# Kernel tuning notes

Hardware: AMD Instinct MI355X
Metric: run time of the kernel (lower is better)

## Reference

```python
import jax, jax.numpy as jnp
import numpy as np


def _gcn_conv(x, W, b, src, dst, n_nodes):
    """PyG-style GCNConv: XW, symmetric deg^-1/2 normalization over edges
    (with self-loops already included in src/dst), scatter-add to targets, + bias."""
    xw = x @ W  # [N, F_out]
    ones = jnp.ones(src.shape[0], dtype=xw.dtype)
    deg = jax.ops.segment_sum(ones, dst, num_segments=n_nodes)  # in-degree incl. self-loops
    dinv = jnp.where(deg > 0, jax.lax.rsqrt(jnp.maximum(deg, 1.0)), 0.0)
    norm = dinv[src] * dinv[dst]                        # [E]
    msgs = xw[src] * norm[:, None]                      # [E, F_out] gather + scale
    out = jax.ops.segment_sum(msgs, dst, num_segments=n_nodes)  # scatter-add
    return out + b


def setup_inputs() -> dict:
    key = jax.random.key(0)
    k1, k2, k3, k4 = jax.random.split(key, 4)
    N, E = 100000, 1600000
    IN, HID, OUT = 128, 64, 64
    x = jax.random.normal(k1, (N, IN), dtype=jnp.float32)
    edge_index = jax.random.randint(k2, (2, E), 0, N, dtype=jnp.int64)
    W1 = jax.random.normal(k3, (IN, HID), dtype=jnp.float32) * (1.0 / np.sqrt(IN))
    b1 = jnp.zeros((HID,), dtype=jnp.float32)
    W2 = jax.random.normal(k4, (HID, OUT), dtype=jnp.float32) * (1.0 / np.sqrt(HID))
    b2 = jnp.zeros((OUT,), dtype=jnp.float32)
    return {"x": x, "edge_index": edge_index, "W1": W1, "b1": b1, "W2": W2, "b2": b2}


def reference(x, edge_index, W1, b1, W2, b2):
    n_nodes = x.shape[0]
    # add self-loops (PyG GCNConv default add_self_loops=True)
    loops = jnp.arange(n_nodes, dtype=edge_index.dtype)
    src = jnp.concatenate([edge_index[0], loops])
    dst = jnp.concatenate([edge_index[1], loops])
    h = _gcn_conv(x, W1, b1, src, dst, n_nodes)
    h = jax.nn.relu(h)
    z = _gcn_conv(h, W2, b2, src, dst, n_nodes)
    return z
```

## Files before the change

kernel.cpp:

```cpp
#include <hip/hip_runtime.h>

#define IN_F 128
#define HID_F 64
#define BKT_SHIFT 9
#define BKT_SIZE 512
#define CHUNK 4096

typedef unsigned short ushort_t;
typedef __attribute__((ext_vector_type(8))) short bf16x8;
typedef __attribute__((ext_vector_type(8))) unsigned short u16x8;
typedef __attribute__((ext_vector_type(4))) float f32x4;

__device__ inline ushort_t f2bf(float f) {
    unsigned u = __float_as_uint(f);
    u += 0x7FFFu + ((u >> 16) & 1u);
    return (ushort_t)(u >> 16);
}
__device__ inline float bf2f(ushort_t u) {
    return __uint_as_float((unsigned)u << 16);
}


__global__ __launch_bounds__(256) void k_hist_pack(const int* __restrict__ dst,
        int* __restrict__ ghist, int E, int nbE,
        const float* __restrict__ W1, const float* __restrict__ W2,
        ushort_t* __restrict__ Bp1, ushort_t* __restrict__ Bp2) {
    int tid = threadIdx.x;
    if ((int)blockIdx.x >= nbE) {
        int id = ((int)blockIdx.x - nbE) * 256 + tid;
        int iw = (id < 8192) ? id : id - 8192;
        int j = iw & 7, lane = (iw >> 3) & 63, t = (iw >> 9) & 3, s = iw >> 11;
        int k = s * 32 + ((lane >> 4) << 3) + j;
        int n = t * 16 + (lane & 15);
        if (id < 8192)        Bp1[iw] = f2bf(W1[k * 64 + n]);
        else if (id < 12288)  Bp2[iw] = f2bf(W2[k * 64 + n]);
        return;
    }
    __shared__ int hist[256];
    hist[tid] = 0;
    __syncthreads();
    int e0 = blockIdx.x * CHUNK, e1 = min(e0 + CHUNK, E);
    for (int e = e0 + tid; e < e1; e += 256)
        atomicAdd(&hist[dst[e] >> BKT_SHIFT], 1);
    __syncthreads();
    ghist[blockIdx.x * 256 + tid] = hist[tid];
}

__global__ __launch_bounds__(256) void k_colscan(int* __restrict__ ghist,
        int* __restrict__ gcount, int nb) {
    __shared__ int s[256];
    int t = threadIdx.x;
    int b = blockIdx.x;
    int j0 = 2 * t, j1 = 2 * t + 1;
    int v0 = (j0 < nb) ? ghist[j0 * 256 + b] : 0;
    int v1 = (j1 < nb) ? ghist[j1 * 256 + b] : 0;
    int p = v0 + v1;
    s[t] = p;
    __syncthreads();
    for (int off = 1; off < 256; off <<= 1) {
        int v = (t >= off) ? s[t - off] : 0;
        __syncthreads();
        s[t] += v;
        __syncthreads();
    }
    int excl = s[t] - p;
    if (j0 < nb) ghist[j0 * 256 + b] = excl;
    if (j1 < nb) ghist[j1 * 256 + b] = excl + v0;
    if (t == 255) gcount[b] = s[255];
}

__global__ __launch_bounds__(256) void k_scatter(const int* __restrict__ src,
        const int* __restrict__ dst, const int* __restrict__ ghist,
        const int* __restrict__ gcount, unsigned* __restrict__ gbin, int E) {
    __shared__ int cur[256];
    __shared__ int s[256];
    int tid = threadIdx.x;
    int gc = gcount[tid];
    s[tid] = gc;
    __syncthreads();
    for (int off = 1; off < 256; off <<= 1) {
        int v = (tid >= off) ? s[tid - off] : 0;
        __syncthreads();
        s[tid] += v;
        __syncthreads();
    }
    cur[tid] = ghist[blockIdx.x * 256 + tid] + (s[tid] - gc);
    __syncthreads();
    int e0 = blockIdx.x * CHUNK, e1 = min(e0 + CHUNK, E);
    for (int e = e0 + tid; e < e1; e += 256) {
        int d = dst[e];
        int b = d >> BKT_SHIFT;
        int p = atomicAdd(&cur[b], 1);
        gbin[p] = ((unsigned)(d & (BKT_SIZE - 1)) << 23) | (unsigned)src[e];
    }
}

__global__ __launch_bounds__(256) void k_fill2(const unsigned* __restrict__ gbin,
        const int* __restrict__ gcount, int* __restrict__ rowptr,
        float* __restrict__ dinv, int* __restrict__ col, int N, int E) {
    __shared__ int cnt[4096];
    __shared__ int s[256];
    int tid = threadIdx.x;
    int b = blockIdx.x;
    int gc = gcount[tid];
    s[tid] = gc;
    __syncthreads();
    for (int off = 1; off < 256; off <<= 1) {
        int v = (tid >= off) ? s[tid - off] : 0;
        __syncthreads();
        s[tid] += v;
        __syncthreads();
    }
    int e0 = (b > 0) ? s[b - 1] : 0;
    int e1 = s[b];
    if (b == 0 && tid == 0) rowptr[N] = E;
    __syncthreads();
    #pragma unroll
    for (int k = 0; k < 16; ++k) cnt[tid + k * 256] = 0;
    __syncthreads();
    for (int e = e0 + tid; e < e1; e += 256) {
        unsigned v = gbin[e];
        atomicAdd(&cnt[((v >> 23) << 3) | ((v >> 14) & 7u)], 1);
    }
    __syncthreads();
    int loc[16];
    int lsum = 0;
    #pragma unroll
    for (int k = 0; k < 16; ++k) { loc[k] = cnt[tid * 16 + k]; lsum += loc[k]; }
    s[tid] = lsum;
    __syncthreads();
    for (int off = 1; off < 256; off <<= 1) {
        int v = (tid >= off) ? s[tid - off] : 0;
        __syncthreads();
        s[tid] += v;
        __syncthreads();
    }
    int run = s[tid] - lsum;
    #pragma unroll
    for (int k = 0; k < 16; ++k) { int t2 = loc[k]; cnt[tid * 16 + k] = run; run += t2; }
    __syncthreads();
    int n0 = b << BKT_SHIFT;
    #pragma unroll
    for (int i = tid; i < BKT_SIZE; i += 256) {
        int n = n0 + i;
        if (n < N) {
            int st = cnt[i * 8];
            int en = (i == BKT_SIZE - 1) ? (e1 - e0) : cnt[(i + 1) * 8];
            rowptr[n] = e0 + st;
            dinv[n] = rsqrtf((float)(en - st) + 1.0f);
        }
    }
    __syncthreads();
    for (int e = e0 + tid; e < e1; e += 256) {
        unsigned v = gbin[e];
        int p = atomicAdd(&cnt[((v >> 23) << 3) | ((v >> 14) & 7u)], 1);
        col[e0 + p] = (int)(v & 0x7FFFFFu);
    }
}

template<int K, typename AT>
__global__ __launch_bounds__(256) void k_gemm_mfma(const AT* __restrict__ A,
        const ushort_t* __restrict__ Bp, const float* __restrict__ dinv,
        ushort_t* __restrict__ out, int N) {
    int wave = threadIdx.x >> 6, lane = threadIdx.x & 63;
    int m = lane & 15, q = lane >> 4;
    int row0 = blockIdx.x * 64 + wave * 16;
    int arow = row0 + m;
    int arowc = (arow < N) ? arow : (N - 1);
    f32x4 acc[4] = {};
    #pragma unroll
    for (int s = 0; s < K / 32; ++s) {
        bf16x8 af;
        if constexpr (sizeof(AT) == 4) {
            const float* ap = (const float*)A + (size_t)arowc * K + s * 32 + q * 8;
            float4 x0 = *(const float4*)ap;
            float4 x1 = *(const float4*)(ap + 4);
            af[0] = (short)f2bf(x0.x); af[1] = (short)f2bf(x0.y);
            af[2] = (short)f2bf(x0.z); af[3] = (short)f2bf(x0.w);
            af[4] = (short)f2bf(x1.x); af[5] = (short)f2bf(x1.y);
            af[6] = (short)f2bf(x1.z); af[7] = (short)f2bf(x1.w);
        } else {
            af = *(const bf16x8*)((const ushort_t*)A + (size_t)arowc * K + s * 32 + q * 8);
        }
        #pragma unroll
        for (int t = 0; t < 4; ++t) {
            bf16x8 bf = *(const bf16x8*)(Bp + (size_t)((s * 4 + t) * 64 + lane) * 8);
            acc[t] = __builtin_amdgcn_mfma_f32_16x16x32_bf16(af, bf, acc[t], 0, 0, 0);
        }
    }
    int orow0 = row0 + q * 4;
    float4 d4 = *(const float4*)(dinv + orow0);
    #pragma unroll
    for (int r = 0; r < 4; ++r) {
        int row = orow0 + r;
        if (row < N) {
            float dn = (r == 0) ? d4.x : (r == 1) ? d4.y : (r == 2) ? d4.z : d4.w;
            #pragma unroll
            for (int t = 0; t < 4; ++t)
                out[(size_t)row * 64 + t * 16 + m] = f2bf(acc[t][r] * dn);
        }
    }
}

__global__ __launch_bounds__(256) void k_agg_gemm(const ushort_t* __restrict__ xws,
        const int* __restrict__ rowptr, const int* __restrict__ col,
        const float* __restrict__ dinv, const float* __restrict__ bias,
        const ushort_t* __restrict__ Bp2, ushort_t* __restrict__ out2, int N) {
    __shared__ ushort_t hl[32][72];
    int tid = threadIdx.x;
    int nl = tid >> 3;
    int i = tid & 7;
    int n0 = blockIdx.x * 32;
    int n = n0 + nl;
    u16x8 hz = {};
    if (n < N) {
        int beg = rowptr[n], end = rowptr[n + 1];
        float dn = dinv[n];
        const ushort_t* base = xws + i * 8;
        u16x8 sv = *(const u16x8*)(base + (size_t)n * 64);
        float a[8];
        #pragma unroll
        for (int k = 0; k < 8; ++k) a[k] = bf2f(sv[k]);
        int e = beg;
        for (; e + 8 <= end; e += 8) {
            int c[8];
            #pragma unroll
            for (int j = 0; j < 8; ++j) c[j] = col[e + j];
            u16x8 v[8];
            #pragma unroll
            for (int j = 0; j < 8; ++j) v[j] = *(const u16x8*)(base + (size_t)c[j] * 64);
            #pragma unroll
            for (int j = 0; j < 8; ++j)
                #pragma unroll
                for (int k = 0; k < 8; ++k) a[k] += bf2f(v[j][k]);
        }
        if (e + 4 <= end) {
            int c[4];
            #pragma unroll
            for (int j = 0; j < 4; ++j) c[j] = col[e + j];
            u16x8 v[4];
            #pragma unroll
            for (int j = 0; j < 4; ++j) v[j] = *(const u16x8*)(base + (size_t)c[j] * 64);
            #pragma unroll
            for (int j = 0; j < 4; ++j)
                #pragma unroll
                for (int k = 0; k < 8; ++k) a[k] += bf2f(v[j][k]);
            e += 4;
        }
        for (; e < end; ++e) {
            u16x8 v = *(const u16x8*)(base + (size_t)col[e] * 64);
            #pragma unroll
            for (int k = 0; k < 8; ++k) a[k] += bf2f(v[k]);
        }
        float4 b0 = *(const float4*)(bias + i * 8);
        float4 b1 = *(const float4*)(bias + i * 8 + 4);
        float r[8];
        r[0] = dn * a[0] + b0.x; r[1] = dn * a[1] + b0.y;
        r[2] = dn * a[2] + b0.z; r[3] = dn * a[3] + b0.w;
        r[4] = dn * a[4] + b1.x; r[5] = dn * a[5] + b1.y;
        r[6] = dn * a[6] + b1.z; r[7] = dn * a[7] + b1.w;
        #pragma unroll
        for (int k = 0; k < 8; ++k) hz[k] = f2bf(fmaxf(r[k], 0.f));
    }
    *(u16x8*)&hl[nl][i * 8] = hz;
    __syncthreads();
    int w = tid >> 6, lane = tid & 63;
    int m = lane & 15, q = lane >> 4;
    int mt = w & 1;
    int nt0 = (w >> 1) << 1;
    f32x4 acc[2] = {};
    #pragma unroll
    for (int s = 0; s < 2; ++s) {
        bf16x8 af = *(const bf16x8*)&hl[mt * 16 + m][s * 32 + q * 8];
        #pragma unroll
        for (int tt = 0; tt < 2; ++tt) {
            bf16x8 bf = *(const bf16x8*)(Bp2 + (size_t)((s * 4 + nt0 + tt) * 64 + lane) * 8);
            acc[tt] = __builtin_amdgcn_mfma_f32_16x16x32_bf16(af, bf, acc[tt], 0, 0, 0);
        }
    }
    int orow0 = n0 + mt * 16 + q * 4;
    float4 d4 = *(const float4*)(dinv + orow0);
    #pragma unroll
    for (int r = 0; r < 4; ++r) {
        int row = orow0 + r;
        if (row < N) {
            float dn = (r == 0) ? d4.x : (r == 1) ? d4.y : (r == 2) ? d4.z : d4.w;
            #pragma unroll
            for (int tt = 0; tt < 2; ++tt)
                out2[(size_t)row * 64 + (nt0 + tt) * 16 + m] = f2bf(acc[tt][r] * dn);
        }
    }
}

__global__ __launch_bounds__(256) void k_aggregate(const ushort_t* __restrict__ xws,
        const int* __restrict__ rowptr, const int* __restrict__ col,
        const float* __restrict__ dinv, const float* __restrict__ bias,
        float* __restrict__ outf, int N) {
    int n = (blockIdx.x * 256 + threadIdx.x) >> 3;
    int i = threadIdx.x & 7;
    if (n >= N) return;
    int beg = rowptr[n], end = rowptr[n + 1];
    float dn = dinv[n];
    const ushort_t* base = xws + i * 8;
    u16x8 sv = *(const u16x8*)(base + (size_t)n * 64);
    float a[8];
    #pragma unroll
    for (int k = 0; k < 8; ++k) a[k] = bf2f(sv[k]);
    int e = beg;
    for (; e + 8 <= end; e += 8) {
        int c[8];
        #pragma unroll
        for (int j = 0; j < 8; ++j) c[j] = col[e + j];
        u16x8 v[8];
        #pragma unroll
        for (int j = 0; j < 8; ++j) v[j] = *(const u16x8*)(base + (size_t)c[j] * 64);
        #pragma unroll
        for (int j = 0; j < 8; ++j)
            #pragma unroll
            for (int k = 0; k < 8; ++k) a[k] += bf2f(v[j][k]);
    }
    if (e + 4 <= end) {
        int c[4];
        #pragma unroll
        for (int j = 0; j < 4; ++j) c[j] = col[e + j];
        u16x8 v[4];
        #pragma unroll
        for (int j = 0; j < 4; ++j) v[j] = *(const u16x8*)(base + (size_t)c[j] * 64);
        #pragma unroll
        for (int j = 0; j < 4; ++j)
            #pragma unroll
            for (int k = 0; k < 8; ++k) a[k] += bf2f(v[j][k]);
        e += 4;
    }
    for (; e < end; ++e) {
        u16x8 v = *(const u16x8*)(base + (size_t)col[e] * 64);
        #pragma unroll
        for (int k = 0; k < 8; ++k) a[k] += bf2f(v[k]);
    }
    float4 b0 = *(const float4*)(bias + i * 8);
    float4 b1 = *(const float4*)(bias + i * 8 + 4);
    float4 o0 = {dn * a[0] + b0.x, dn * a[1] + b0.y, dn * a[2] + b0.z, dn * a[3] + b0.w};
    float4 o1 = {dn * a[4] + b1.x, dn * a[5] + b1.y, dn * a[6] + b1.z, dn * a[7] + b1.w};
    *(float4*)(outf + (size_t)n * 64 + i * 8) = o0;
    *(float4*)(outf + (size_t)n * 64 + i * 8 + 4) = o1;
}


extern "C" void kernel_launch(void* const* d_in, const int* in_sizes, int n_in,
                              void* d_out, int out_size, void* d_ws, size_t ws_size,
                              hipStream_t stream) {
    const float* x  = (const float*)d_in[0];
    const int*   ei = (const int*)d_in[1];
    const float* W1 = (const float*)d_in[2];
    const float* b1 = (const float*)d_in[3];
    const float* W2 = (const float*)d_in[4];
    const float* b2 = (const float*)d_in[5];
    float* out = (float*)d_out;

    const int N = in_sizes[0] / IN_F;
    const int E = in_sizes[1] / 2;
    const int* src = ei;
    const int* dst = ei + E;

    char* ws = (char*)d_ws;
    const size_t MB = 1u << 20;
    int*      gcount  = (int*)     (ws + 12288);
    ushort_t* Bp1     = (ushort_t*)(ws + 16384);
    ushort_t* Bp2     = (ushort_t*)(ws + 49152);
    int*      rowptr  = (int*)     (ws + 1 * MB);
    float*    dinv    = (float*)   (ws + 2 * MB);
    unsigned* gbin    = (unsigned*)(ws + 3 * MB);
    int*      ghist   = (int*)     (ws + 10 * MB);
    int*      col     = (int*)     (ws + 11 * MB);
    ushort_t* xws     = (ushort_t*)(ws + 20 * MB);
    ushort_t* xws2    = (ushort_t*)(ws + 36 * MB);

    const int nbE = (E + CHUNK - 1) / CHUNK;
    const int nbB = (N + BKT_SIZE - 1) / BKT_SIZE;
    const int nbG = (N + 63) / 64;
    const int nbA = (N * 8 + 255) / 256;

    k_hist_pack<<<nbE + 48, 256, 0, stream>>>(dst, ghist, E, nbE, W1, W2, Bp1, Bp2);
    k_colscan<<<256, 256, 0, stream>>>(ghist, gcount, nbE);
    k_scatter<<<nbE, 256, 0, stream>>>(src, dst, ghist, gcount, gbin, E);
    k_fill2  <<<nbB, 256, 0, stream>>>(gbin, gcount, rowptr, dinv, col, N, E);

    k_gemm_mfma<IN_F, float><<<nbG, 256, 0, stream>>>(x, Bp1, dinv, xws, N);
    k_agg_gemm<<<nbA, 256, 0, stream>>>(xws, rowptr, col, dinv, b1, Bp2, xws2, N);
    k_aggregate<<<nbA, 256, 0, stream>>>(xws2, rowptr, col, dinv, b2, out, N);
}
```

Baseline: 223.2 us.

## Overlap first-layer GEMM with CSR build by moving source-side normalization into aggregation

The first GEMM no longer scales its output by dinv, so it can run before the degrees are known. Its blocks are folded into the colscan and scatter launches as extra blocks, so the GEMM overlaps the graph-sorting stages and one launch is dropped. The source-side dinv scaling moves into the first aggregation as a per-edge gather of dinv[c]. This adds an extra 4-byte random load and a multiply per edge, and it lengthens the colscan and scatter kernels.

```diff
diff --git a/kernel.cpp b/kernel.cpp
--- a/kernel.cpp
+++ b/kernel.cpp
@@ -18,6 +18,43 @@
 }
 __device__ inline float bf2f(ushort_t u) {
     return __uint_as_float((unsigned)u << 16);
+}
+
+__device__ inline void gemm1_block(int gb, const float* __restrict__ A,
+        const ushort_t* __restrict__ Bp, ushort_t* __restrict__ out, int N) {
+    int tid = threadIdx.x;
+    int wave = tid >> 6, lane = tid & 63;
+    int m = lane & 15, q = lane >> 4;
+    int row0 = gb * 64 + wave * 16;
+    int arow = row0 + m;
+    int arowc = (arow < N) ? arow : (N - 1);
+    f32x4 acc[4] = {};
+    #pragma unroll
+    for (int s = 0; s < 4; ++s) {
+        const float* ap = A + (size_t)arowc * 128 + s * 32 + q * 8;
+        float4 x0 = *(const float4*)ap;
+        float4 x1 = *(const float4*)(ap + 4);
+        bf16x8 af;
+        af[0] = (short)f2bf(x0.x); af[1] = (short)f2bf(x0.y);
+        af[2] = (short)f2bf(x0.z); af[3] = (short)f2bf(x0.w);
+        af[4] = (short)f2bf(x1.x); af[5] = (short)f2bf(x1.y);
+        af[6] = (short)f2bf(x1.z); af[7] = (short)f2bf(x1.w);
+        #pragma unroll
+        for (int t = 0; t < 4; ++t) {
+            bf16x8 bf = *(const bf16x8*)(Bp + (size_t)((s * 4 + t) * 64 + lane) * 8);
+            acc[t] = __builtin_amdgcn_mfma_f32_16x16x32_bf16(af, bf, acc[t], 0, 0, 0);
+        }
+    }
+    int orow0 = row0 + q * 4;
+    #pragma unroll
+    for (int r = 0; r < 4; ++r) {
+        int row = orow0 + r;
+        if (row < N) {
+            #pragma unroll
+            for (int t = 0; t < 4; ++t)
+                out[(size_t)row * 64 + t * 16 + m] = f2bf(acc[t][r]);
+        }
+    }
 }
 
 
@@ -47,7 +84,13 @@
 }
 
 __global__ __launch_bounds__(256) void k_colscan(int* __restrict__ ghist,
-        int* __restrict__ gcount, int nb) {
+        int* __restrict__ gcount, int nb,
+        const float* __restrict__ x, const ushort_t* __restrict__ Bp1,
+        ushort_t* __restrict__ xw, int N, int gbase) {
+    if ((int)blockIdx.x >= 256) {
+        gemm1_block(gbase + (int)blockIdx.x - 256, x, Bp1, xw, N);
+        return;
+    }
     __shared__ int s[256];
     int t = threadIdx.x;
     int b = blockIdx.x;
@@ -71,7 +114,13 @@
 
 __global__ __launch_bounds__(256) void k_scatter(const int* __restrict__ src,
         const int* __restrict__ dst, const int* __restrict__ ghist,
-        const int* __restrict__ gcount, unsigned* __restrict__ gbin, int E) {
+        const int* __restrict__ gcount, unsigned* __restrict__ gbin, int E, int nbE,
+        const float* __restrict__ x, const ushort_t* __restrict__ Bp1,
+        ushort_t* __restrict__ xw, int N, int gbase) {
+    if ((int)blockIdx.x >= nbE) {
+        gemm1_block(gbase + (int)blockIdx.x - nbE, x, Bp1, xw, N);
+        return;
+    }
     __shared__ int cur[256];
     __shared__ int s[256];
     int tid = threadIdx.x;
@@ -158,51 +207,7 @@
     }
 }
 
-template<int K, typename AT>
-__global__ __launch_bounds__(256) void k_gemm_mfma(const AT* __restrict__ A,
-        const ushort_t* __restrict__ Bp, const float* __restrict__ dinv,
-        ushort_t* __restrict__ out, int N) {
-    int wave = threadIdx.x >> 6, lane = threadIdx.x & 63;
-    int m = lane & 15, q = lane >> 4;
-    int row0 = blockIdx.x * 64 + wave * 16;
-    int arow = row0 + m;
-    int arowc = (arow < N) ? arow : (N - 1);
-    f32x4 acc[4] = {};
-    #pragma unroll
-    for (int s = 0; s < K / 32; ++s) {
-        bf16x8 af;
-        if constexpr (sizeof(AT) == 4) {
-            const float* ap = (const float*)A + (size_t)arowc * K + s * 32 + q * 8;
-            float4 x0 = *(const float4*)ap;
-            float4 x1 = *(const float4*)(ap + 4);
-            af[0] = (short)f2bf(x0.x); af[1] = (short)f2bf(x0.y);
-            af[2] = (short)f2bf(x0.z); af[3] = (short)f2bf(x0.w);
-            af[4] = (short)f2bf(x1.x); af[5] = (short)f2bf(x1.y);
-            af[6] = (short)f2bf(x1.z); af[7] = (short)f2bf(x1.w);
-        } else {
-            af = *(const bf16x8*)((const ushort_t*)A + (size_t)arowc * K + s * 32 + q * 8);
-        }
-        #pragma unroll
-        for (int t = 0; t < 4; ++t) {
-            bf16x8 bf = *(const bf16x8*)(Bp + (size_t)((s * 4 + t) * 64 + lane) * 8);
-            acc[t] = __builtin_amdgcn_mfma_f32_16x16x32_bf16(af, bf, acc[t], 0, 0, 0);
-        }
-    }
-    int orow0 = row0 + q * 4;
-    float4 d4 = *(const float4*)(dinv + orow0);
-    #pragma unroll
-    for (int r = 0; r < 4; ++r) {
-        int row = orow0 + r;
-        if (row < N) {
-            float dn = (r == 0) ? d4.x : (r == 1) ? d4.y : (r == 2) ? d4.z : d4.w;
-            #pragma unroll
-            for (int t = 0; t < 4; ++t)
-                out[(size_t)row * 64 + t * 16 + m] = f2bf(acc[t][r] * dn);
-        }
-    }
-}
-
-__global__ __launch_bounds__(256) void k_agg_gemm(const ushort_t* __restrict__ xws,
+__global__ __launch_bounds__(256) void k_agg_gemm(const ushort_t* __restrict__ xw,
         const int* __restrict__ rowptr, const int* __restrict__ col,
         const float* __restrict__ dinv, const float* __restrict__ bias,
         const ushort_t* __restrict__ Bp2, ushort_t* __restrict__ out2, int N) {
@@ -216,41 +221,49 @@
     if (n < N) {
         int beg = rowptr[n], end = rowptr[n + 1];
         float dn = dinv[n];
-        const ushort_t* base = xws + i * 8;
+        const ushort_t* base = xw + i * 8;
         u16x8 sv = *(const u16x8*)(base + (size_t)n * 64);
         float a[8];
         #pragma unroll
-        for (int k = 0; k < 8; ++k) a[k] = bf2f(sv[k]);
+        for (int k = 0; k < 8; ++k) a[k] = bf2f(sv[k]) * dn;
         int e = beg;
         for (; e + 8 <= end; e += 8) {
             int c[8];
             #pragma unroll
             for (int j = 0; j < 8; ++j) c[j] = col[e + j];
+            float dv[8];
+            #pragma unroll
+            for (int j = 0; j < 8; ++j) dv[j] = dinv[c[j]];
             u16x8 v[8];
             #pragma unroll
             for (int j = 0; j < 8; ++j) v[j] = *(const u16x8*)(base + (size_t)c[j] * 64);
             #pragma unroll
             for (int j = 0; j < 8; ++j)
                 #pragma unroll
-                for (int k = 0; k < 8; ++k) a[k] += bf2f(v[j][k]);
+                for (int k = 0; k < 8; ++k) a[k] += bf2f(v[j][k]) * dv[j];
         }
         if (e + 4 <= end) {
             int c[4];
             #pragma unroll
             for (int j = 0; j < 4; ++j) c[j] = col[e + j];
+            float dv[4];
+            #pragma unroll
+            for (int j = 0; j < 4; ++j) dv[j] = dinv[c[j]];
             u16x8 v[4];
             #pragma unroll
             for (int j = 0; j < 4; ++j) v[j] = *(const u16x8*)(base + (size_t)c[j] * 64);
             #pragma unroll
             for (int j = 0; j < 4; ++j)
                 #pragma unroll
-                for (int k = 0; k < 8; ++k) a[k] += bf2f(v[j][k]);
+                for (int k = 0; k < 8; ++k) a[k] += bf2f(v[j][k]) * dv[j];
             e += 4;
         }
         for (; e < end; ++e) {
-            u16x8 v = *(const u16x8*)(base + (size_t)col[e] * 64);
-            #pragma unroll
-            for (int k = 0; k < 8; ++k) a[k] += bf2f(v[k]);
+            int c = col[e];
+            float dv = dinv[c];
+            u16x8 v = *(const u16x8*)(base + (size_t)c * 64);
+            #pragma unroll
+            for (int k = 0; k < 8; ++k) a[k] += bf2f(v[k]) * dv;
         }
         float4 b0 = *(const float4*)(bias + i * 8);
         float4 b1 = *(const float4*)(bias + i * 8 + 4);
@@ -372,7 +385,7 @@
     unsigned* gbin    = (unsigned*)(ws + 3 * MB);
     int*      ghist   = (int*)     (ws + 10 * MB);
     int*      col     = (int*)     (ws + 11 * MB);
-    ushort_t* xws     = (ushort_t*)(ws + 20 * MB);
+    ushort_t* xw      = (ushort_t*)(ws + 20 * MB);
     ushort_t* xws2    = (ushort_t*)(ws + 36 * MB);
 
     const int nbE = (E + CHUNK - 1) / CHUNK;
@@ -380,12 +393,15 @@
     const int nbG = (N + 63) / 64;
     const int nbA = (N * 8 + 255) / 256;
 
+    const int g0 = (nbG < 300) ? nbG : 300;
+    const int g1 = nbG - g0;
+
     k_hist_pack<<<nbE + 48, 256, 0, stream>>>(dst, ghist, E, nbE, W1, W2, Bp1, Bp2);
-    k_colscan<<<256, 256, 0, stream>>>(ghist, gcount, nbE);
-    k_scatter<<<nbE, 256, 0, stream>>>(src, dst, ghist, gcount, gbin, E);
+    k_colscan<<<256 + g0, 256, 0, stream>>>(ghist, gcount, nbE, x, Bp1, xw, N, 0);
+    k_scatter<<<nbE + g1, 256, 0, stream>>>(src, dst, ghist, gcount, gbin, E, nbE,
+                                            x, Bp1, xw, N, g0);
     k_fill2  <<<nbB, 256, 0, stream>>>(gbin, gcount, rowptr, dinv, col, N, E);
 
-    k_gemm_mfma<IN_F, float><<<nbG, 256, 0, stream>>>(x, Bp1, dinv, xws, N);
-    k_agg_gemm<<<nbA, 256, 0, stream>>>(xws, rowptr, col, dinv, b1, Bp2, xws2, N);
+    k_agg_gemm<<<nbA, 256, 0, stream>>>(xw, rowptr, col, dinv, b1, Bp2, xws2, N);
     k_aggregate<<<nbA, 256, 0, stream>>>(xws2, rowptr, col, dinv, b2, out, N);
 }
```

After: 231.3 us. 1.04x slower.
